# Kernel optimization log

Hardware: AMD Instinct MI355X
Metric: run time of the kernel (lower is better)

Reference implementation:

```python
import jax, jax.numpy as jnp
import numpy as np

N = 50000
D = 256
H = 128
L = 64
V = 3
E = 1600000
P = 10000


def setup_inputs() -> dict:
    key = jax.random.key(0)
    ks = jax.random.split(key, 10)
    X = jax.random.normal(ks[0], (N, D), dtype=jnp.float32)
    # row-normalize features, mimicking preprocess_features
    X = X / (jnp.sum(jnp.abs(X), axis=1, keepdims=True) + 1e-8)
    edge_idx = jax.random.randint(ks[1], (V, E, 2), 0, N, dtype=jnp.int32)
    edge_vals = jax.random.uniform(ks[2], (V, E), dtype=jnp.float32) / 32.0  # ~normalized adj weights
    W = jax.random.normal(ks[3], (V, D, H), dtype=jnp.float32) / np.sqrt(D)
    b = jnp.zeros((V, H), dtype=jnp.float32)
    Wmu = jax.random.normal(ks[4], (V * H, L), dtype=jnp.float32) / np.sqrt(V * H)
    bmu = jnp.zeros((L,), dtype=jnp.float32)
    Wsig = jax.random.normal(ks[5], (V * H, L), dtype=jnp.float32) / np.sqrt(V * H)
    bsig = jnp.zeros((L,), dtype=jnp.float32)
    pos_edges = jax.random.randint(ks[6], (P, 2), 0, N, dtype=jnp.int32)
    neg_edges = jax.random.randint(ks[7], (P, 2), 0, N, dtype=jnp.int32)
    return {"X": X, "edge_idx": edge_idx, "edge_vals": edge_vals, "W": W, "b": b,
            "Wmu": Wmu, "bmu": bmu, "Wsig": Wsig, "bsig": bsig,
            "pos_edges": pos_edges, "neg_edges": neg_edges}


def _energy_kl(mu, sigma, pairs):
    # pairs: [P,2]; KL(N_j || N_i) style energy as in graph2gauss
    mu_i = mu[pairs[:, 0]]          # [P,L]
    mu_j = mu[pairs[:, 1]]
    sig_i = sigma[pairs[:, 0]]
    sig_j = sigma[pairs[:, 1]]
    ratio = sig_j / sig_i           # [P,L]
    trace_fac = jnp.sum(ratio, axis=1)
    log_det = jnp.sum(jnp.log(ratio + 1e-14), axis=1)
    mu_diff_sq = jnp.sum(jnp.square(mu_i - mu_j) / sig_i, axis=1)
    return 0.5 * (trace_fac + mu_diff_sq - L - log_det)


def reference(X, edge_idx, edge_vals, W, b, Wmu, bmu, Wsig, bsig, pos_edges, neg_edges):
    # Per-view sparse GCN layer: relu(A_v @ (X @ W_v) + b_v)
    XW = jnp.einsum('nd,vdh->vnh', X, W)  # [V,N,H]

    def view_conv(xw, idx, vals, bv):
        src, dst = idx[:, 0], idx[:, 1]
        msgs = vals[:, None] * xw[src]                          # [E,H] gather
        agg = jax.ops.segment_sum(msgs, dst, num_segments=N)    # [N,H] scatter-add
        return jax.nn.relu(agg + bv)

    h = jax.vmap(view_conv)(XW, edge_idx, edge_vals, b)  # [V,N,H]
    # concat views along feature dim (reduce=None)
    concat = jnp.transpose(h, (1, 0, 2)).reshape(N, V * H)  # [N, V*H]

    # Gaussian encoder (non_linear=True): mu linear; sigma = elu(...) + 1 + eps > 0
    mu = concat @ Wmu + bmu
    sigma = jax.nn.elu(concat @ Wsig + bsig) + 1.0 + 1e-14

    eng_pos = _energy_kl(mu, sigma, pos_edges)
    eng_neg = _energy_kl(mu, sigma, neg_edges)
    energy = jnp.square(eng_pos) + jnp.exp(-eng_neg)
    return jnp.mean(energy)
```

## Files before the change

kernel.cpp:

```cpp
#include <hip/hip_runtime.h>
#include <hip/hip_fp16.h>

#define N_NODES 50000
#define DIM 256
#define HID 128
#define LAT 64
#define NV 3
#define NE 1600000
#define NP 10000
#define NBUCK 196
#define BIN_CHUNK 4096
#define STAGE2 12288
#define EWAVES 1000

typedef short v8s __attribute__((ext_vector_type(8)));
typedef float v4f __attribute__((ext_vector_type(4)));

__device__ __forceinline__ unsigned f2bf1(float f) {
  unsigned x = __float_as_uint(f);
  return (x + 0x7fffu + ((x >> 16) & 1u)) >> 16;
}
__device__ __forceinline__ unsigned pack2bf(float a, float b) {
  return (f2bf1(a) & 0xffffu) | (f2bf1(b) << 16);
}

__global__ __launch_bounds__(256) void k_wt(const float* __restrict__ W,
                                            const float* __restrict__ Wmu,
                                            const float* __restrict__ Wsig,
                                            unsigned short* __restrict__ WtA,
                                            unsigned short* __restrict__ Wt2) {
  int t = blockIdx.x * 256 + threadIdx.x;
  if (t < NV * HID * DIM) {
    int d = t & 255, vh = t >> 8;
    int h = vh & 127, v = vh >> 7;
    WtA[t] = (unsigned short)f2bf1(W[((size_t)v * DIM + d) * HID + h]);
  }
  int t2 = t - NV * HID * DIM;
  if (t2 >= 0 && t2 < HID * (NV * HID)) {
    int k = t2 % 384, o = t2 / 384;
    float w = (o < 64) ? Wmu[(size_t)k * 64 + o] : Wsig[(size_t)k * 64 + (o - 64)];
    Wt2[t2] = (unsigned short)f2bf1(w);
  }
}

#define BM1 32
__global__ __launch_bounds__(192) void k_gemm_xw(const float* __restrict__ X,
                                                 const unsigned short* __restrict__ WtA,
                                                 unsigned short* __restrict__ XWh) {
  const int nbase = blockIdx.x * BM1;
  const int tid = threadIdx.x;
  const int lane = tid & 63, wv = tid >> 6;
  __shared__ unsigned short Xs[BM1 * 256];
#pragma unroll
  for (int i = 0; i < 6; i++) {
    int task = i * 192 + tid;
    if (task < BM1 * 32) {
      int r = task >> 5, g = task & 31;
      int n = nbase + r;
      float4 x0 = make_float4(0.f, 0.f, 0.f, 0.f), x1 = x0;
      if (n < N_NODES) {
        const float4* xp = reinterpret_cast<const float4*>(X + (size_t)n * DIM + g * 8);
        x0 = xp[0]; x1 = xp[1];
      }
      int gp = g ^ (r & 7);
      uint4 u;
      u.x = pack2bf(x0.x, x0.y); u.y = pack2bf(x0.z, x0.w);
      u.z = pack2bf(x1.x, x1.y); u.w = pack2bf(x1.z, x1.w);
      *reinterpret_cast<uint4*>(&Xs[r * 256 + gp * 8]) = u;
    }
  }
  __syncthreads();
  const unsigned short* Wv = WtA + (size_t)wv * HID * DIM;
  const int bcol = lane & 15, bk = lane >> 4;
  v4f acc[2][8];
#pragma unroll
  for (int mt = 0; mt < 2; mt++)
#pragma unroll
    for (int nt = 0; nt < 8; nt++)
#pragma unroll
      for (int q = 0; q < 4; q++) acc[mt][nt][q] = 0.f;
  for (int ks = 0; ks < 8; ks++) {
    v8s B[8];
#pragma unroll
    for (int nt = 0; nt < 8; nt++)
      B[nt] = *reinterpret_cast<const v8s*>(Wv + (size_t)(nt * 16 + bcol) * DIM + ks * 32 + bk * 8);
#pragma unroll
    for (int mt = 0; mt < 2; mt++) {
      int r = mt * 16 + bcol;
      int g = ks * 4 + bk;
      v8s A = *reinterpret_cast<const v8s*>(&Xs[r * 256 + (g ^ (r & 7)) * 8]);
#pragma unroll
      for (int nt = 0; nt < 8; nt++)
        acc[mt][nt] = __builtin_amdgcn_mfma_f32_16x16x32_bf16(A, B[nt], acc[mt][nt], 0, 0, 0);
    }
  }
  unsigned short* out = XWh + (size_t)wv * N_NODES * HID;
#pragma unroll
  for (int mt = 0; mt < 2; mt++)
#pragma unroll
    for (int rr = 0; rr < 4; rr++) {
      int n = nbase + mt * 16 + bk * 4 + rr;
      if (n < N_NODES) {
#pragma unroll
        for (int nt = 0; nt < 8; nt++)
          out[(size_t)n * HID + nt * 16 + bcol] = (unsigned short)f2bf1(acc[mt][nt][rr]);
      }
    }
}

__global__ __launch_bounds__(256) void k_bhist(const int* __restrict__ edge_idx,
                                               int* __restrict__ gcount) {
  const int v = blockIdx.y;
  const int tid = threadIdx.x;
  __shared__ int h[NBUCK];
  if (tid < NBUCK) h[tid] = 0;
  __syncthreads();
  const int2* ei = reinterpret_cast<const int2*>(edge_idx) + (size_t)v * NE;
  const int stride = gridDim.x * 256;
  for (int e = blockIdx.x * 256 + tid; e < NE; e += stride) {
    atomicAdd(&h[ei[e].y >> 8], 1);
  }
  __syncthreads();
  if (tid < NBUCK && h[tid]) atomicAdd(&gcount[v * NBUCK + tid], h[tid]);
}

__global__ __launch_bounds__(640) void k_bscan(const int* __restrict__ gcount,
                                               int* __restrict__ bbase,
                                               int* __restrict__ bcur) {
  __shared__ int x[NV * NBUCK];
  const int tid = threadIdx.x;
  const int v = (tid < NV * NBUCK) ? (tid / NBUCK) : 0;
  int c = 0;
  if (tid < NV * NBUCK) { c = gcount[tid]; x[tid] = c; }
  __syncthreads();
  for (int off = 1; off < NV * NBUCK; off <<= 1) {
    int t = 0;
    if (tid < NV * NBUCK && tid - off >= v * NBUCK) t = x[tid - off];
    __syncthreads();
    if (tid < NV * NBUCK) x[tid] += t;
    __syncthreads();
  }
  if (tid < NV * NBUCK) {
    int excl = x[tid] - c;
    int base = v * NE + excl;
    bbase[tid] = base;
    bcur[tid] = base;
  }
}

__global__ __launch_bounds__(256) void k_bin(const int* __restrict__ edge_idx,
                                             const float* __restrict__ edge_vals,
                                             int* __restrict__ bcur,
                                             uint2* __restrict__ spack8) {
  const int v = blockIdx.y;
  const int tid = threadIdx.x;
  const int lane = tid & 63, wv = tid >> 6;
  __shared__ uint2 buf[BIN_CHUNK];
  __shared__ unsigned short bid[BIN_CHUNK];
  __shared__ int lcount[NBUCK];
  __shared__ int loffs[NBUCK];
  __shared__ int gbase[NBUCK];
  __shared__ int wsum[4];
  if (tid < NBUCK) lcount[tid] = 0;
  __syncthreads();

  const int ebase = blockIdx.x * BIN_CHUNK;
  const int2* ei = reinterpret_cast<const int2*>(edge_idx) + (size_t)v * NE;
  const float* ev = edge_vals + (size_t)v * NE;

  unsigned px[16];
  int sdy[16];
  int rk[16];
#pragma unroll
  for (int i = 0; i < 16; i++) {
    int e = ebase + i * 256 + tid;
    bool ok = e < NE;
    int2 sd = ok ? ei[e] : make_int2(0, 0);
    float val = ok ? ev[e] : 0.f;
    px[i] = (((unsigned)sd.x) << 16) | (unsigned)__half_as_ushort(__float2half(val));
    sdy[i] = sd.y;
    rk[i] = ok ? atomicAdd(&lcount[sd.y >> 8], 1) : 0;
  }
  __syncthreads();
  {
    int c = (tid < NBUCK) ? lcount[tid] : 0;
    int s = c;
#pragma unroll
    for (int off = 1; off < 64; off <<= 1) {
      int t = __shfl_up(s, off);
      if (lane >= off) s += t;
    }
    if ((tid & 63) == 63) wsum[wv] = s;
    __syncthreads();
    int pre = 0;
#pragma unroll
    for (int w = 0; w < 4; w++) pre += (w < wv) ? wsum[w] : 0;
    if (tid < NBUCK) loffs[tid] = pre + s - c;
    __syncthreads();
    if (tid < NBUCK) gbase[tid] = atomicAdd(&bcur[v * NBUCK + tid], lcount[tid]);
  }
  __syncthreads();
#pragma unroll
  for (int i = 0; i < 16; i++) {
    int e = ebase + i * 256 + tid;
    if (e < NE) {
      int bkt = sdy[i] >> 8;
      int slot = loffs[bkt] + rk[i];
      buf[slot] = make_uint2(px[i], (unsigned)(sdy[i] & 255));
      bid[slot] = (unsigned short)bkt;
    }
  }
  __syncthreads();
  const int total = loffs[NBUCK - 1] + lcount[NBUCK - 1];
  for (int s = tid; s < total; s += 256) {
    int bkt = bid[s];
    uint2 q = buf[s];
    spack8[(size_t)gbase[bkt] + (s - loffs[bkt])] = q;
  }
}

__global__ __launch_bounds__(1024) void k_sort2(const int* __restrict__ gcount,
                                                const int* __restrict__ bbase,
                                                const uint2* __restrict__ spack8,
                                                unsigned* __restrict__ csr,
                                                int* __restrict__ counts_g,
                                                int* __restrict__ offsets_g) {
  const int b = blockIdx.x, v = blockIdx.y;
  const int tid = threadIdx.x;
  __shared__ unsigned buf[STAGE2];
  __shared__ int h[256], cur[256];
  __shared__ int wsum[4];
  if (tid < 256) h[tid] = 0;
  __syncthreads();
  const int cnt = gcount[v * NBUCK + b];
  const int base = bbase[v * NBUCK + b];
  const uint2* ep = spack8 + base;
  for (int i = tid; i < cnt; i += 1024) atomicAdd(&h[ep[i].y], 1);
  __syncthreads();
  {
    const int lane = tid & 63, wv = tid >> 6;
    int c = (tid < 256) ? h[tid] : 0;
    int s = c;
#pragma unroll
    for (int off = 1; off < 64; off <<= 1) {
      int t = __shfl_up(s, off);
      if (lane >= off) s += t;
    }
    if (tid < 256 && lane == 63) wsum[wv] = s;
    __syncthreads();
    if (tid < 256) {
      int pre = 0;
#pragma unroll
      for (int w = 0; w < 4; w++) pre += (w < wv) ? wsum[w] : 0;
      int excl = pre + s - c;
      cur[tid] = excl;
      int n = (b << 8) + tid;
      if (n < N_NODES) {
        counts_g[v * N_NODES + n] = c;
        offsets_g[v * N_NODES + n] = base + excl;
      }
    }
  }
  __syncthreads();
  for (int i = tid; i < cnt; i += 1024) {
    uint2 q = ep[i];
    int r = atomicAdd(&cur[q.y], 1);
    if (r < STAGE2) buf[r] = q.x;
    else csr[(size_t)base + r] = q.x;
  }
  __syncthreads();
  const int m = min(cnt, STAGE2);
  for (int s = tid; s < m; s += 1024) csr[(size_t)base + s] = buf[s];
}

__global__ __launch_bounds__(256) void k_agg(const int* __restrict__ counts_g,
                                             const int* __restrict__ offsets_g,
                                             const unsigned* __restrict__ csr,
                                             const unsigned* __restrict__ XWu,
                                             const float* __restrict__ b,
                                             unsigned* __restrict__ cat) {
  const int v = blockIdx.y;
  const int wave = threadIdx.x >> 6;
  const int lane = threadIdx.x & 63;
  const int n = blockIdx.x * 4 + wave;
  if (n >= N_NODES) return;
  const int cnt = counts_g[v * N_NODES + n];
  const unsigned* pp = csr + offsets_g[v * N_NODES + n];
  const unsigned* xw = XWu + (size_t)v * N_NODES * 64;
  float a0 = 0.f, a1 = 0.f;
  for (int c0 = 0; c0 < cnt; c0 += 64) {
    const int m = min(64, cnt - c0);
    unsigned p = (lane < m) ? pp[c0 + lane] : 0u;
    for (int jb = 0; jb < m; jb += 16) {
      unsigned u[16];
      float vals[16];
#pragma unroll
      for (int k = 0; k < 16; k++) {
        unsigned pj = (unsigned)__shfl((int)p, jb + k);
        vals[k] = __half2float(__ushort_as_half((unsigned short)(pj & 0xffffu)));
        u[k] = xw[(size_t)(pj >> 16) * 64 + lane];
      }
#pragma unroll
      for (int k = 0; k < 16; k++) {
        a0 += vals[k] * __uint_as_float(u[k] << 16);
        a1 += vals[k] * __uint_as_float(u[k] & 0xffff0000u);
      }
    }
  }
  float h0 = a0 + b[v * HID + 2 * lane];
  float h1 = a1 + b[v * HID + 2 * lane + 1];
  h0 = h0 > 0.f ? h0 : 0.f;
  h1 = h1 > 0.f ? h1 : 0.f;
  cat[(size_t)n * 192 + v * 64 + lane] = pack2bf(h0, h1);
}

__global__ __launch_bounds__(256) void k_musig(const unsigned short* __restrict__ catus,
                                               const unsigned short* __restrict__ Wt2,
                                               const float* __restrict__ bmu,
                                               const float* __restrict__ bsig,
                                               float* __restrict__ mu,
                                               float* __restrict__ sig) {
  const int nbase = blockIdx.x * 64;
  const int tid = threadIdx.x;
  const int lane = tid & 63, wv = tid >> 6;
  __shared__ unsigned short Cs[64 * 384];
#pragma unroll
  for (int i = 0; i < 12; i++) {
    int task = i * 256 + tid;
    int r = task / 48, g = task % 48;
    int n = nbase + r;
    uint4 u = make_uint4(0u, 0u, 0u, 0u);
    if (n < N_NODES) u = *reinterpret_cast<const uint4*>(catus + (size_t)n * 384 + g * 8);
    int gp = (g & ~7) | ((g & 7) ^ (r & 7));
    *reinterpret_cast<uint4*>(&Cs[r * 384 + gp * 8]) = u;
  }
  __syncthreads();
  const int bcol = lane & 15, bk = lane >> 4;
  v4f acc[8];
#pragma unroll
  for (int nt = 0; nt < 8; nt++)
#pragma unroll
    for (int q = 0; q < 4; q++) acc[nt][q] = 0.f;
  for (int ks = 0; ks < 12; ks++) {
    v8s B[8];
#pragma unroll
    for (int nt = 0; nt < 8; nt++)
      B[nt] = *reinterpret_cast<const v8s*>(Wt2 + (size_t)(nt * 16 + bcol) * 384 + ks * 32 + bk * 8);
    int r = wv * 16 + bcol;
    int g = ks * 4 + bk;
    int gp = (g & ~7) | ((g & 7) ^ (r & 7));
    v8s A = *reinterpret_cast<const v8s*>(&Cs[r * 384 + gp * 8]);
#pragma unroll
    for (int nt = 0; nt < 8; nt++)
      acc[nt] = __builtin_amdgcn_mfma_f32_16x16x32_bf16(A, B[nt], acc[nt], 0, 0, 0);
  }
#pragma unroll
  for (int rr = 0; rr < 4; rr++) {
    int n = nbase + wv * 16 + bk * 4 + rr;
    if (n < N_NODES) {
#pragma unroll
      for (int nt = 0; nt < 8; nt++) {
        int o = nt * 16 + bcol;
        float val = acc[nt][rr];
        if (o < 64) {
          mu[(size_t)n * 64 + o] = val + bmu[o];
        } else {
          float s = val + bsig[o - 64];
          float e = (s > 0.f) ? s : (__expf(s) - 1.f);
          sig[(size_t)n * 64 + (o - 64)] = e + 1.f + 1e-14f;
        }
      }
    }
  }
}

__global__ __launch_bounds__(256) void k_energy1(const float* __restrict__ mu,
                                                 const float* __restrict__ sig,
                                                 const int* __restrict__ pos_e,
                                                 const int* __restrict__ neg_e,
                                                 float* __restrict__ partial) {
  const int lane = threadIdx.x & 63;
  const int gw = blockIdx.x * 4 + (threadIdx.x >> 6);
  float accum = 0.f;
  int t = gw;
  int2 pr = make_int2(0, 0);
  if (t < 2 * NP)
    pr = (t < NP) ? reinterpret_cast<const int2*>(pos_e)[t]
                  : reinterpret_cast<const int2*>(neg_e)[t - NP];
  for (; t < 2 * NP; t += EWAVES) {
    const bool ispos = t < NP;
    const int tn = t + EWAVES;
    int2 nxt = make_int2(0, 0);
    if (tn < 2 * NP)
      nxt = (tn < NP) ? reinterpret_cast<const int2*>(pos_e)[tn]
                      : reinterpret_cast<const int2*>(neg_e)[tn - NP];
    float mi = mu[(size_t)pr.x * 64 + lane], mj = mu[(size_t)pr.y * 64 + lane];
    float si = sig[(size_t)pr.x * 64 + lane], sj = sig[(size_t)pr.y * 64 + lane];
    float ratio = sj / si;
    float t1 = ratio;
    float t2 = __logf(ratio + 1e-14f);
    float d = mi - mj;
    float t3 = d * d / si;
#pragma unroll
    for (int off = 32; off; off >>= 1) {
      t1 += __shfl_xor(t1, off);
      t2 += __shfl_xor(t2, off);
      t3 += __shfl_xor(t3, off);
    }
    float eng = 0.5f * (t1 + t3 - 64.f - t2);
    accum += ispos ? (eng * eng) : __expf(-eng);
    pr = nxt;
  }
  if (lane == 0) partial[gw] = accum;
}

__global__ __launch_bounds__(256) void k_ered(const float* __restrict__ partial,
                                              float* __restrict__ out) {
  const int tid = threadIdx.x;
  const int lane = tid & 63, wv = tid >> 6;
  __shared__ float ws_[4];
  float s = 0.f;
  for (int i = tid; i < EWAVES; i += 256) s += partial[i];
#pragma unroll
  for (int off = 32; off; off >>= 1) s += __shfl_xor(s, off);
  if (lane == 0) ws_[wv] = s;
  __syncthreads();
  if (tid == 0) out[0] = (ws_[0] + ws_[1] + ws_[2] + ws_[3]) * (1.f / NP);
}

extern "C" void kernel_launch(void* const* d_in, const int* in_sizes, int n_in,
                              void* d_out, int out_size, void* d_ws, size_t ws_size,
                              hipStream_t stream) {
  const float* X = (const float*)d_in[0];
  const int* edge_idx = (const int*)d_in[1];
  const float* edge_vals = (const float*)d_in[2];
  const float* W = (const float*)d_in[3];
  const float* b = (const float*)d_in[4];
  const float* Wmu = (const float*)d_in[5];
  const float* bmu = (const float*)d_in[6];
  const float* Wsig = (const float*)d_in[7];
  const float* bsig = (const float*)d_in[8];
  const int* pos_e = (const int*)d_in[9];
  const int* neg_e = (const int*)d_in[10];
  float* out = (float*)d_out;

  char* ws = (char*)d_ws;
  const size_t o_xw    = 0;
  const size_t o_cat   = 38400000;
  const size_t o_sp8   = 76800000;
  const size_t o_csr   = 115200000;
  const size_t o_cntg  = 134400000;
  const size_t o_offg  = 135000000;
  const size_t o_gcnt  = 135600000;
  const size_t o_bbase = 135604096;
  const size_t o_bcur  = 135608192;
  const size_t o_wta   = 135612288;
  const size_t o_wt2   = 135808896;
  const size_t o_part  = 135907200;
  const size_t total   = 135911200;
  const size_t o_mu    = o_sp8;
  const size_t o_sig   = o_sp8 + 12800000;
  if (ws_size < total) return;

  unsigned short* XWh = (unsigned short*)(ws + o_xw);
  unsigned* XWu = (unsigned*)(ws + o_xw);
  unsigned* cat = (unsigned*)(ws + o_cat);
  unsigned short* catus = (unsigned short*)(ws + o_cat);
  uint2* spack8 = (uint2*)(ws + o_sp8);
  unsigned* csr = (unsigned*)(ws + o_csr);
  int* counts_g = (int*)(ws + o_cntg);
  int* offsets_g = (int*)(ws + o_offg);
  int* gcount = (int*)(ws + o_gcnt);
  int* bbase = (int*)(ws + o_bbase);
  int* bcur = (int*)(ws + o_bcur);
  unsigned short* WtA = (unsigned short*)(ws + o_wta);
  unsigned short* Wt2 = (unsigned short*)(ws + o_wt2);
  float* partial = (float*)(ws + o_part);
  float* mu = (float*)(ws + o_mu);
  float* sig = (float*)(ws + o_sig);

  hipMemsetAsync(gcount, 0, NV * NBUCK * sizeof(int), stream);

  hipLaunchKernelGGL(k_wt, dim3((NV * HID * DIM + HID * 384 + 255) / 256), dim3(256), 0,
                     stream, W, Wmu, Wsig, WtA, Wt2);
  hipLaunchKernelGGL(k_gemm_xw, dim3((N_NODES + BM1 - 1) / BM1), dim3(192), 0, stream,
                     X, WtA, XWh);
  hipLaunchKernelGGL(k_bhist, dim3(256, NV), dim3(256), 0, stream, edge_idx, gcount);
  hipLaunchKernelGGL(k_bscan, dim3(1), dim3(640), 0, stream, gcount, bbase, bcur);
  hipLaunchKernelGGL(k_bin, dim3((NE + BIN_CHUNK - 1) / BIN_CHUNK, NV), dim3(256), 0,
                     stream, edge_idx, edge_vals, bcur, spack8);
  hipLaunchKernelGGL(k_sort2, dim3(NBUCK, NV), dim3(1024), 0, stream,
                     gcount, bbase, spack8, csr, counts_g, offsets_g);
  hipLaunchKernelGGL(k_agg, dim3((N_NODES + 3) / 4, NV), dim3(256), 0, stream,
                     counts_g, offsets_g, csr, XWu, b, cat);
  hipLaunchKernelGGL(k_musig, dim3((N_NODES + 63) / 64), dim3(256), 0, stream,
                     catus, Wt2, bmu, bsig, mu, sig);
  hipLaunchKernelGGL(k_energy1, dim3(EWAVES / 4), dim3(256), 0, stream,
                     mu, sig, pos_e, neg_e, partial);
  hipLaunchKernelGGL(k_ered, dim3(1), dim3(256), 0, stream, partial, out);
}
```

Before: 348.0 us.

## Store XW intermediate in FP8 and gather it in aggregation

The GEMM now writes X@W as scaled FP8 (×64) instead of bf16, halving the bytes of the table that the sparse aggregation gathers per edge. The aggregation kernel is restructured to read packed edge entries directly per 16-edge chunk rather than shuffling them across lanes, unpacks FP8 pairs with the hardware convert instruction, and rescales at the end. This lowers gather bandwidth and workspace size at the cost of reduced precision in the intermediate features, which may affect accuracy.

```diff
diff --git a/kernel.cpp b/kernel.cpp
--- a/kernel.cpp
+++ b/kernel.cpp
@@ -15,6 +15,7 @@
 
 typedef short v8s __attribute__((ext_vector_type(8)));
 typedef float v4f __attribute__((ext_vector_type(4)));
+typedef float v2f __attribute__((ext_vector_type(2)));
 
 __device__ __forceinline__ unsigned f2bf1(float f) {
   unsigned x = __float_as_uint(f);
@@ -46,7 +47,7 @@
 #define BM1 32
 __global__ __launch_bounds__(192) void k_gemm_xw(const float* __restrict__ X,
                                                  const unsigned short* __restrict__ WtA,
-                                                 unsigned short* __restrict__ XWh) {
+                                                 unsigned char* __restrict__ XW8) {
   const int nbase = blockIdx.x * BM1;
   const int tid = threadIdx.x;
   const int lane = tid & 63, wv = tid >> 6;
@@ -94,7 +95,7 @@
         acc[mt][nt] = __builtin_amdgcn_mfma_f32_16x16x32_bf16(A, B[nt], acc[mt][nt], 0, 0, 0);
     }
   }
-  unsigned short* out = XWh + (size_t)wv * N_NODES * HID;
+  unsigned char* out = XW8 + (size_t)wv * N_NODES * 128;
 #pragma unroll
   for (int mt = 0; mt < 2; mt++)
 #pragma unroll
@@ -102,8 +103,10 @@
       int n = nbase + mt * 16 + bk * 4 + rr;
       if (n < N_NODES) {
 #pragma unroll
-        for (int nt = 0; nt < 8; nt++)
-          out[(size_t)n * HID + nt * 16 + bcol] = (unsigned short)f2bf1(acc[mt][nt][rr]);
+        for (int nt = 0; nt < 8; nt++) {
+          int r8 = __builtin_amdgcn_cvt_pk_fp8_f32(acc[mt][nt][rr] * 64.f, 0.f, 0, false);
+          out[(size_t)n * 128 + nt * 16 + bcol] = (unsigned char)(r8 & 0xff);
+        }
       }
     }
 }
@@ -276,7 +279,7 @@
 __global__ __launch_bounds__(256) void k_agg(const int* __restrict__ counts_g,
                                              const int* __restrict__ offsets_g,
                                              const unsigned* __restrict__ csr,
-                                             const unsigned* __restrict__ XWu,
+                                             const unsigned char* __restrict__ XW8,
                                              const float* __restrict__ b,
                                              unsigned* __restrict__ cat) {
   const int v = blockIdx.y;
@@ -286,29 +289,47 @@
   if (n >= N_NODES) return;
   const int cnt = counts_g[v * N_NODES + n];
   const unsigned* pp = csr + offsets_g[v * N_NODES + n];
-  const unsigned* xw = XWu + (size_t)v * N_NODES * 64;
+  const unsigned char* xw = XW8 + (size_t)v * N_NODES * 128 + lane * 2;
   float a0 = 0.f, a1 = 0.f;
-  for (int c0 = 0; c0 < cnt; c0 += 64) {
-    const int m = min(64, cnt - c0);
-    unsigned p = (lane < m) ? pp[c0 + lane] : 0u;
-    for (int jb = 0; jb < m; jb += 16) {
-      unsigned u[16];
-      float vals[16];
-#pragma unroll
-      for (int k = 0; k < 16; k++) {
-        unsigned pj = (unsigned)__shfl((int)p, jb + k);
-        vals[k] = __half2float(__ushort_as_half((unsigned short)(pj & 0xffffu)));
-        u[k] = xw[(size_t)(pj >> 16) * 64 + lane];
+  int c0 = 0;
+  for (; c0 + 16 <= cnt; c0 += 16) {
+    unsigned pj[16];
+#pragma unroll
+    for (int k = 0; k < 16; k++) pj[k] = pp[c0 + k];
+    unsigned short u[16];
+#pragma unroll
+    for (int k = 0; k < 16; k++)
+      u[k] = *reinterpret_cast<const unsigned short*>(xw + ((size_t)(pj[k] >> 16) << 7));
+#pragma unroll
+    for (int k = 0; k < 16; k++) {
+      float val = __half2float(__ushort_as_half((unsigned short)(pj[k] & 0xffffu)));
+      v2f f = __builtin_amdgcn_cvt_pk_f32_fp8((int)(unsigned)u[k], false);
+      a0 += val * f[0];
+      a1 += val * f[1];
+    }
+  }
+  if (c0 < cnt) {
+    unsigned pj[16];
+#pragma unroll
+    for (int k = 0; k < 16; k++) pj[k] = pp[c0 + k];
+    unsigned short u[16];
+#pragma unroll
+    for (int k = 0; k < 16; k++)
+      u[k] = (c0 + k < cnt)
+                 ? *reinterpret_cast<const unsigned short*>(xw + ((size_t)(pj[k] >> 16) << 7))
+                 : (unsigned short)0;
+#pragma unroll
+    for (int k = 0; k < 16; k++) {
+      if (c0 + k < cnt) {
+        float val = __half2float(__ushort_as_half((unsigned short)(pj[k] & 0xffffu)));
+        v2f f = __builtin_amdgcn_cvt_pk_f32_fp8((int)(unsigned)u[k], false);
+        a0 += val * f[0];
+        a1 += val * f[1];
       }
-#pragma unroll
-      for (int k = 0; k < 16; k++) {
-        a0 += vals[k] * __uint_as_float(u[k] << 16);
-        a1 += vals[k] * __uint_as_float(u[k] & 0xffff0000u);
-      }
-    }
-  }
-  float h0 = a0 + b[v * HID + 2 * lane];
-  float h1 = a1 + b[v * HID + 2 * lane + 1];
+    }
+  }
+  float h0 = a0 * 0.015625f + b[v * HID + 2 * lane];
+  float h1 = a1 * 0.015625f + b[v * HID + 2 * lane + 1];
   h0 = h0 > 0.f ? h0 : 0.f;
   h1 = h1 > 0.f ? h1 : 0.f;
   cat[(size_t)n * 192 + v * 64 + lane] = pack2bf(h0, h1);
@@ -446,24 +467,23 @@
 
   char* ws = (char*)d_ws;
   const size_t o_xw    = 0;
-  const size_t o_cat   = 38400000;
-  const size_t o_sp8   = 76800000;
-  const size_t o_csr   = 115200000;
-  const size_t o_cntg  = 134400000;
-  const size_t o_offg  = 135000000;
-  const size_t o_gcnt  = 135600000;
-  const size_t o_bbase = 135604096;
-  const size_t o_bcur  = 135608192;
-  const size_t o_wta   = 135612288;
-  const size_t o_wt2   = 135808896;
-  const size_t o_part  = 135907200;
-  const size_t total   = 135911200;
+  const size_t o_cat   = 19200000;
+  const size_t o_sp8   = 57600000;
+  const size_t o_csr   = 96000000;
+  const size_t o_cntg  = 115200000;
+  const size_t o_offg  = 115800000;
+  const size_t o_gcnt  = 116400000;
+  const size_t o_bbase = 116404096;
+  const size_t o_bcur  = 116408192;
+  const size_t o_wta   = 116412288;
+  const size_t o_wt2   = 116608896;
+  const size_t o_part  = 116707200;
+  const size_t total   = 116711200;
   const size_t o_mu    = o_sp8;
   const size_t o_sig   = o_sp8 + 12800000;
   if (ws_size < total) return;
 
-  unsigned short* XWh = (unsigned short*)(ws + o_xw);
-  unsigned* XWu = (unsigned*)(ws + o_xw);
+  unsigned char* XW8 = (unsigned char*)(ws + o_xw);
   unsigned* cat = (unsigned*)(ws + o_cat);
   unsigned short* catus = (unsigned short*)(ws + o_cat);
   uint2* spack8 = (uint2*)(ws + o_sp8);
@@ -484,7 +504,7 @@
   hipLaunchKernelGGL(k_wt, dim3((NV * HID * DIM + HID * 384 + 255) / 256), dim3(256), 0,
                      stream, W, Wmu, Wsig, WtA, Wt2);
   hipLaunchKernelGGL(k_gemm_xw, dim3((N_NODES + BM1 - 1) / BM1), dim3(192), 0, stream,
-                     X, WtA, XWh);
+                     X, WtA, XW8);
   hipLaunchKernelGGL(k_bhist, dim3(256, NV), dim3(256), 0, stream, edge_idx, gcount);
   hipLaunchKernelGGL(k_bscan, dim3(1), dim3(640), 0, stream, gcount, bbase, bcur);
   hipLaunchKernelGGL(k_bin, dim3((NE + BIN_CHUNK - 1) / BIN_CHUNK, NV), dim3(256), 0,
@@ -492,7 +512,7 @@
   hipLaunchKernelGGL(k_sort2, dim3(NBUCK, NV), dim3(1024), 0, stream,
                      gcount, bbase, spack8, csr, counts_g, offsets_g);
   hipLaunchKernelGGL(k_agg, dim3((N_NODES + 3) / 4, NV), dim3(256), 0, stream,
-                     counts_g, offsets_g, csr, XWu, b, cat);
+                     counts_g, offsets_g, csr, XW8, b, cat);
   hipLaunchKernelGGL(k_musig, dim3((N_NODES + 63) / 64), dim3(256), 0, stream,
                      catus, Wt2, bmu, bsig, mu, sig);
   hipLaunchKernelGGL(k_energy1, dim3(EWAVES / 4), dim3(256), 0, stream,
```

Result: faster. 321.7 us (-7.5%).
